# Kernel optimization log

Measured on AMD Instinct MI355X. Metric: run time of the kernel, lower is better.

Reference implementation:

```python
import jax, jax.numpy as jnp
import numpy as np

EMB_DIM = 256
N_EMBED = 1024
BETA = 0.25


def setup_inputs() -> dict:
    key = jax.random.key(0)
    k1, k2 = jax.random.split(key)
    encoderout = jax.random.normal(k1, (32, EMB_DIM, 32, 32), dtype=jnp.float32)
    # embedding.weight.data.normal_(mean=0, std=1/n_embed)
    codebook = jax.random.normal(k2, (N_EMBED, EMB_DIM), dtype=jnp.float32) * (1.0 / N_EMBED)
    return {"encoderout": encoderout, "codebook": codebook}


def reference(encoderout, codebook):
    # NCHW -> NHWC
    x = jnp.transpose(encoderout, (0, 2, 3, 1))  # [B,H,W,D]
    flat = x.reshape(-1, EMB_DIM)                # [N,D]
    d2 = (jnp.sum(flat * flat, axis=1, keepdims=True)
          + jnp.sum(codebook * codebook, axis=1)[None, :]
          - 2.0 * flat @ codebook.T)             # [N,K]
    idx = jnp.argmin(d2, axis=1)                 # [N]
    quant = codebook[idx].reshape(x.shape)       # [B,H,W,D]
    codebook_loss = jnp.mean((quant - jax.lax.stop_gradient(x)) ** 2)
    commitment_loss = jnp.mean((x - jax.lax.stop_gradient(quant)) ** 2)
    loss = codebook_loss + BETA * commitment_loss
    # FAITHFUL to source bug: straight-through output is overwritten by the
    # input permuted back to NCHW, so out == encoderout.
    out = jnp.transpose(x, (0, 3, 1, 2))
    return (out, loss, codebook_loss, commitment_loss)
```

## Files before the change

### kernel.cpp

```cpp
#include <hip/hip_runtime.h>
#include <stdint.h>

typedef short s8v __attribute__((ext_vector_type(8)));
typedef float f4v __attribute__((ext_vector_type(4)));

#define EMB_DIM 256
#define HW      1024
#define NROWS   32768
#define NELEM   (NROWS * EMB_DIM)

#define PK_OFF   0u
#define CBN_OFF  524288u
#define PSQ_OFF  528384u
#define PSM_OFF  530432u

__device__ __forceinline__ unsigned f2bf(float f) {
    union { float f; unsigned u; } c; c.f = f;
    unsigned u = c.u;
    return (u + 0x7FFFu + ((u >> 16) & 1u)) >> 16;
}

__global__ __launch_bounds__(256) void prep_cb(const float* __restrict__ cb,
                                               unsigned short* __restrict__ pk,
                                               float* __restrict__ cbn) {
    int T = blockIdx.x, t = threadIdx.x;
    {
        int code = t >> 4, seg = t & 15;
        const float* src = cb + (size_t)(T * 16 + code) * EMB_DIM + seg * 16;
        float s2 = 0.f;
        #pragma unroll
        for (int k = 0; k < 4; ++k) {
            float4 v = *(const float4*)(src + 4 * k);
            s2 += v.x * v.x + v.y * v.y + v.z * v.z + v.w * v.w;
        }
        #pragma unroll
        for (int m = 1; m < 16; m <<= 1) s2 += __shfl_xor(s2, m, 64);
        if (seg == 0) cbn[T * 16 + code] = s2;
    }
    #pragma unroll
    for (int it = 0; it < 2; ++it) {
        int idx = t + 256 * it;
        int s = idx >> 6, l = idx & 63, G = l >> 4, ci = l & 15;
        const float* q = cb + (size_t)(T * 16 + ci) * EMB_DIM + 32 * s + 8 * G;
        float4 v0 = *(const float4*)(q);
        float4 v1 = *(const float4*)(q + 4);
        unsigned o0 = f2bf(v0.x) | (f2bf(v0.y) << 16);
        unsigned o1 = f2bf(v0.z) | (f2bf(v0.w) << 16);
        unsigned o2 = f2bf(v1.x) | (f2bf(v1.y) << 16);
        unsigned o3 = f2bf(v1.z) | (f2bf(v1.w) << 16);
        *(uint4*)((char*)pk + (size_t)T * 8192 + (size_t)idx * 16) =
            make_uint4(o0, o1, o2, o3);
    }
}

__global__ __launch_bounds__(256, 2) void vq_fused(const float* __restrict__ x,
                                                   float* __restrict__ out,
                                                   const unsigned short* __restrict__ pk,
                                                   const float* __restrict__ cbn,
                                                   float* __restrict__ psq,
                                                   float* __restrict__ psm) {
    __shared__ float smemf[64 * 69];
    __shared__ uint4 frag[4 * 8 * 64];
    __shared__ float mloc[4][64];
    __shared__ float red[4];

    int t = threadIdx.x;
    int blk = blockIdx.x;
    int b = blk >> 4, p0 = (blk & 15) << 6;
    const float* xb = x   + (size_t)b * (EMB_DIM * HW) + p0;
    float*       ob = out + (size_t)b * (EMB_DIM * HW) + p0;

    int l = t & 63, w = t >> 6;
    int G = l >> 4, ci = l & 15;

    float sq = 0.f;
    int pq = t & 15, dd = t >> 4;
    for (int kd = 0; kd < 4; ++kd) {
        #pragma unroll
        for (int c2 = 0; c2 < 4; ++c2) {
            int dl = dd + 16 * c2;
            size_t off = (size_t)(kd * 64 + dl) * HW + 4 * pq;
            float4 v = *(const float4*)(xb + off);
            *(float4*)(ob + off) = v;
            sq += v.x * v.x + v.y * v.y + v.z * v.z + v.w * v.w;
            float* dst = &smemf[dl * 69 + 4 * pq];
            dst[0] = v.x; dst[1] = v.y; dst[2] = v.z; dst[3] = v.w;
        }
        __syncthreads();
        #pragma unroll
        for (int it = 0; it < 2; ++it) {
            int f = t + 256 * it;
            int fl = f & 63, sL = (f >> 6) & 1, R = f >> 7;
            int fG = fl >> 4, fci = fl & 15;
            const float* q = &smemf[(32 * sL + 8 * fG) * 69 + 16 * R + fci];
            unsigned o0 = f2bf(q[0])   | (f2bf(q[69])  << 16);
            unsigned o1 = f2bf(q[138]) | (f2bf(q[207]) << 16);
            unsigned o2 = f2bf(q[276]) | (f2bf(q[345]) << 16);
            unsigned o3 = f2bf(q[414]) | (f2bf(q[483]) << 16);
            frag[(R * 8 + 2 * kd + sL) * 64 + fl] = make_uint4(o0, o1, o2, o3);
        }
        __syncthreads();
    }
    #pragma unroll
    for (int m = 1; m < 64; m <<= 1) sq += __shfl_xor(sq, m, 64);
    if (l == 0) red[w] = sq;

    s8v a[4][8];
    #pragma unroll
    for (int R = 0; R < 4; ++R)
        #pragma unroll
        for (int s = 0; s < 8; ++s)
            a[R][s] = *(const s8v*)&frag[(R * 8 + s) * 64 + l];

    float mv[4][4];
    #pragma unroll
    for (int R = 0; R < 4; ++R)
        #pragma unroll
        for (int r = 0; r < 4; ++r) mv[R][r] = 1e30f;

    const char* pb = (const char*)pk + (size_t)(w * 16) * 8192 + (size_t)l * 16;
    #pragma unroll 2
    for (int T = 0; T < 16; ++T) {
        const char* pt = pb + (size_t)T * 8192;
        f4v ac0 = {0.f,0.f,0.f,0.f}, ac1 = {0.f,0.f,0.f,0.f};
        f4v ac2 = {0.f,0.f,0.f,0.f}, ac3 = {0.f,0.f,0.f,0.f};
        #pragma unroll
        for (int s = 0; s < 8; ++s) {
            s8v bf = *(const s8v*)(pt + s * 1024);
            ac0 = __builtin_amdgcn_mfma_f32_16x16x32_bf16(a[0][s], bf, ac0, 0, 0, 0);
            ac1 = __builtin_amdgcn_mfma_f32_16x16x32_bf16(a[1][s], bf, ac1, 0, 0, 0);
            ac2 = __builtin_amdgcn_mfma_f32_16x16x32_bf16(a[2][s], bf, ac2, 0, 0, 0);
            ac3 = __builtin_amdgcn_mfma_f32_16x16x32_bf16(a[3][s], bf, ac3, 0, 0, 0);
        }
        float cv = cbn[(w * 16 + T) * 16 + ci];
        #pragma unroll
        for (int r = 0; r < 4; ++r) {
            mv[0][r] = fminf(mv[0][r], cv - 2.f * ac0[r]);
            mv[1][r] = fminf(mv[1][r], cv - 2.f * ac1[r]);
            mv[2][r] = fminf(mv[2][r], cv - 2.f * ac2[r]);
            mv[3][r] = fminf(mv[3][r], cv - 2.f * ac3[r]);
        }
    }

    #pragma unroll
    for (int R = 0; R < 4; ++R)
        #pragma unroll
        for (int r = 0; r < 4; ++r) {
            float v = mv[R][r];
            #pragma unroll
            for (int m = 1; m < 16; m <<= 1) v = fminf(v, __shfl_xor(v, m, 64));
            mv[R][r] = v;
        }
    if (ci == 0) {
        #pragma unroll
        for (int R = 0; R < 4; ++R)
            #pragma unroll
            for (int r = 0; r < 4; ++r)
                mloc[w][16 * R + 4 * G + r] = mv[R][r];
    }
    __syncthreads();

    if (t < 64) {
        float m = fminf(fminf(mloc[0][t], mloc[1][t]),
                        fminf(mloc[2][t], mloc[3][t]));
        #pragma unroll
        for (int mm = 1; mm < 64; mm <<= 1) m += __shfl_xor(m, mm, 64);
        if (t == 0) {
            psm[blk] = m;
            psq[blk] = red[0] + red[1] + red[2] + red[3];
        }
    }
}

__global__ __launch_bounds__(512) void fin_kernel(const float* __restrict__ psm,
                                                  const float* __restrict__ psq,
                                                  float* __restrict__ out) {
    int t = threadIdx.x;
    double s = (double)psm[t] + (double)psq[t];
    #pragma unroll
    for (int m = 1; m < 64; m <<= 1) s += __shfl_xor(s, m, 64);
    __shared__ double ds[8];
    if ((t & 63) == 0) ds[t >> 6] = s;
    __syncthreads();
    if (t == 0) {
        double tot = 0.0;
        #pragma unroll
        for (int k = 0; k < 8; ++k) tot += ds[k];
        double cl = tot / (double)NELEM;
        out[NELEM + 0] = (float)(1.25 * cl);
        out[NELEM + 1] = (float)cl;
        out[NELEM + 2] = (float)cl;
    }
}

extern "C" void kernel_launch(void* const* d_in, const int* in_sizes, int n_in,
                              void* d_out, int out_size, void* d_ws, size_t ws_size,
                              hipStream_t stream) {
    const float* enc = (const float*)d_in[0];
    const float* cb  = (const float*)d_in[1];
    float* out = (float*)d_out;

    unsigned short* pk = (unsigned short*)((char*)d_ws + PK_OFF);
    float* cbn = (float*)((char*)d_ws + CBN_OFF);
    float* psq = (float*)((char*)d_ws + PSQ_OFF);
    float* psm = (float*)((char*)d_ws + PSM_OFF);

    prep_cb<<<64, 256, 0, stream>>>(cb, pk, cbn);
    vq_fused<<<512, 256, 0, stream>>>(enc, out, pk, cbn, psq, psm);
    fin_kernel<<<1, 512, 0, stream>>>(psm, psq, out);
}
```

Measured before the change: 108.0 us.

## Prefetch codebook tiles, stagger tile order, nontemporal copy, fuse final reduction

The codebook MFMA loop now double-buffers its B fragments, loading the next tile into registers while the current one is consumed. Each block starts at a different tile offset to spread L2 accesses. The input-to-output copy uses nontemporal loads and stores. The separate finalize kernel is replaced by a last-block-done atomic counter inside the main kernel, which removes one launch but adds register pressure and a fence/atomic per block.

```diff
diff --git a/kernel.cpp b/kernel.cpp
--- a/kernel.cpp
+++ b/kernel.cpp
@@ -13,6 +13,7 @@
 #define CBN_OFF  524288u
 #define PSQ_OFF  528384u
 #define PSM_OFF  530432u
+#define DONE_OFF 532480u
 
 __device__ __forceinline__ unsigned f2bf(float f) {
     union { float f; unsigned u; } c; c.f = f;
@@ -22,8 +23,10 @@
 
 __global__ __launch_bounds__(256) void prep_cb(const float* __restrict__ cb,
                                                unsigned short* __restrict__ pk,
-                                               float* __restrict__ cbn) {
+                                               float* __restrict__ cbn,
+                                               unsigned* __restrict__ done) {
     int T = blockIdx.x, t = threadIdx.x;
+    if (T == 0 && t == 0) *done = 0u;
     {
         int code = t >> 4, seg = t & 15;
         const float* src = cb + (size_t)(T * 16 + code) * EMB_DIM + seg * 16;
@@ -58,11 +61,14 @@
                                                    const unsigned short* __restrict__ pk,
                                                    const float* __restrict__ cbn,
                                                    float* __restrict__ psq,
-                                                   float* __restrict__ psm) {
+                                                   float* __restrict__ psm,
+                                                   unsigned* __restrict__ done) {
     __shared__ float smemf[64 * 69];
     __shared__ uint4 frag[4 * 8 * 64];
     __shared__ float mloc[4][64];
     __shared__ float red[4];
+    __shared__ bool  lastf;
+    __shared__ double dred[4];
 
     int t = threadIdx.x;
     int blk = blockIdx.x;
@@ -80,8 +86,8 @@
         for (int c2 = 0; c2 < 4; ++c2) {
             int dl = dd + 16 * c2;
             size_t off = (size_t)(kd * 64 + dl) * HW + 4 * pq;
-            float4 v = *(const float4*)(xb + off);
-            *(float4*)(ob + off) = v;
+            f4v v = __builtin_nontemporal_load((const f4v*)(xb + off));
+            __builtin_nontemporal_store(v, (f4v*)(ob + off));
             sq += v.x * v.x + v.y * v.y + v.z * v.z + v.w * v.w;
             float* dst = &smemf[dl * 69 + 4 * pq];
             dst[0] = v.x; dst[1] = v.y; dst[2] = v.z; dst[3] = v.w;
@@ -118,21 +124,33 @@
         #pragma unroll
         for (int r = 0; r < 4; ++r) mv[R][r] = 1e30f;
 
-    const char* pb = (const char*)pk + (size_t)(w * 16) * 8192 + (size_t)l * 16;
+    const char* lbase = (const char*)pk + (size_t)l * 16;
+    int qbase = w * 16;
+    int off = blk & 15;
+    s8v cur[8], nxt[8];
+    {
+        const char* pt = lbase + (size_t)(qbase + off) * 8192;
+        #pragma unroll
+        for (int s = 0; s < 8; ++s) cur[s] = *(const s8v*)(pt + (size_t)s * 1024);
+    }
     #pragma unroll 2
-    for (int T = 0; T < 16; ++T) {
-        const char* pt = pb + (size_t)T * 8192;
+    for (int i = 0; i < 16; ++i) {
+        int Tn = qbase + ((off + ((i + 1) & 15)) & 15);
+        const char* pn = lbase + (size_t)Tn * 8192;
+        #pragma unroll
+        for (int s = 0; s < 8; ++s) nxt[s] = *(const s8v*)(pn + (size_t)s * 1024);
+
         f4v ac0 = {0.f,0.f,0.f,0.f}, ac1 = {0.f,0.f,0.f,0.f};
         f4v ac2 = {0.f,0.f,0.f,0.f}, ac3 = {0.f,0.f,0.f,0.f};
         #pragma unroll
         for (int s = 0; s < 8; ++s) {
-            s8v bf = *(const s8v*)(pt + s * 1024);
-            ac0 = __builtin_amdgcn_mfma_f32_16x16x32_bf16(a[0][s], bf, ac0, 0, 0, 0);
-            ac1 = __builtin_amdgcn_mfma_f32_16x16x32_bf16(a[1][s], bf, ac1, 0, 0, 0);
-            ac2 = __builtin_amdgcn_mfma_f32_16x16x32_bf16(a[2][s], bf, ac2, 0, 0, 0);
-            ac3 = __builtin_amdgcn_mfma_f32_16x16x32_bf16(a[3][s], bf, ac3, 0, 0, 0);
-        }
-        float cv = cbn[(w * 16 + T) * 16 + ci];
+            ac0 = __builtin_amdgcn_mfma_f32_16x16x32_bf16(a[0][s], cur[s], ac0, 0, 0, 0);
+            ac1 = __builtin_amdgcn_mfma_f32_16x16x32_bf16(a[1][s], cur[s], ac1, 0, 0, 0);
+            ac2 = __builtin_amdgcn_mfma_f32_16x16x32_bf16(a[2][s], cur[s], ac2, 0, 0, 0);
+            ac3 = __builtin_amdgcn_mfma_f32_16x16x32_bf16(a[3][s], cur[s], ac3, 0, 0, 0);
+        }
+        int Tc = qbase + ((off + i) & 15);
+        float cv = cbn[Tc * 16 + ci];
         #pragma unroll
         for (int r = 0; r < 4; ++r) {
             mv[0][r] = fminf(mv[0][r], cv - 2.f * ac0[r]);
@@ -140,6 +158,8 @@
             mv[2][r] = fminf(mv[2][r], cv - 2.f * ac2[r]);
             mv[3][r] = fminf(mv[3][r], cv - 2.f * ac3[r]);
         }
+        #pragma unroll
+        for (int s = 0; s < 8; ++s) cur[s] = nxt[s];
     }
 
     #pragma unroll
@@ -166,30 +186,37 @@
         #pragma unroll
         for (int mm = 1; mm < 64; mm <<= 1) m += __shfl_xor(m, mm, 64);
         if (t == 0) {
-            psm[blk] = m;
-            psq[blk] = red[0] + red[1] + red[2] + red[3];
-        }
-    }
-}
-
-__global__ __launch_bounds__(512) void fin_kernel(const float* __restrict__ psm,
-                                                  const float* __restrict__ psq,
-                                                  float* __restrict__ out) {
-    int t = threadIdx.x;
-    double s = (double)psm[t] + (double)psq[t];
-    #pragma unroll
-    for (int m = 1; m < 64; m <<= 1) s += __shfl_xor(s, m, 64);
-    __shared__ double ds[8];
-    if ((t & 63) == 0) ds[t >> 6] = s;
+            __hip_atomic_store(&psm[blk], m, __ATOMIC_RELAXED, __HIP_MEMORY_SCOPE_AGENT);
+            __hip_atomic_store(&psq[blk], red[0] + red[1] + red[2] + red[3],
+                               __ATOMIC_RELAXED, __HIP_MEMORY_SCOPE_AGENT);
+            __threadfence();
+            unsigned old = __hip_atomic_fetch_add(done, 1u, __ATOMIC_RELAXED,
+                                                  __HIP_MEMORY_SCOPE_AGENT);
+            lastf = (old == 511u);
+        }
+    }
     __syncthreads();
-    if (t == 0) {
-        double tot = 0.0;
-        #pragma unroll
-        for (int k = 0; k < 8; ++k) tot += ds[k];
-        double cl = tot / (double)NELEM;
-        out[NELEM + 0] = (float)(1.25 * cl);
-        out[NELEM + 1] = (float)cl;
-        out[NELEM + 2] = (float)cl;
+
+    if (lastf) {
+        __threadfence();
+        double s = 0.0;
+        #pragma unroll
+        for (int h = 0; h < 2; ++h) {
+            int idx = t + 256 * h;
+            s += (double)__hip_atomic_load(&psm[idx], __ATOMIC_RELAXED, __HIP_MEMORY_SCOPE_AGENT)
+               + (double)__hip_atomic_load(&psq[idx], __ATOMIC_RELAXED, __HIP_MEMORY_SCOPE_AGENT);
+        }
+        #pragma unroll
+        for (int m = 1; m < 64; m <<= 1) s += __shfl_xor(s, m, 64);
+        if (l == 0) dred[w] = s;
+        __syncthreads();
+        if (t == 0) {
+            double tot = dred[0] + dred[1] + dred[2] + dred[3];
+            double cl = tot / (double)NELEM;
+            out[NELEM + 0] = (float)(1.25 * cl);
+            out[NELEM + 1] = (float)cl;
+            out[NELEM + 2] = (float)cl;
+        }
     }
 }
 
@@ -201,11 +228,11 @@
     float* out = (float*)d_out;
 
     unsigned short* pk = (unsigned short*)((char*)d_ws + PK_OFF);
-    float* cbn = (float*)((char*)d_ws + CBN_OFF);
-    float* psq = (float*)((char*)d_ws + PSQ_OFF);
-    float* psm = (float*)((char*)d_ws + PSM_OFF);
-
-    prep_cb<<<64, 256, 0, stream>>>(cb, pk, cbn);
-    vq_fused<<<512, 256, 0, stream>>>(enc, out, pk, cbn, psq, psm);
-    fin_kernel<<<1, 512, 0, stream>>>(psm, psq, out);
-}
+    float* cbn  = (float*)((char*)d_ws + CBN_OFF);
+    float* psq  = (float*)((char*)d_ws + PSQ_OFF);
+    float* psm  = (float*)((char*)d_ws + PSM_OFF);
+    unsigned* done = (unsigned*)((char*)d_ws + DONE_OFF);
+
+    prep_cb<<<64, 256, 0, stream>>>(cb, pk, cbn, done);
+    vq_fused<<<512, 256, 0, stream>>>(enc, out, pk, cbn, psq, psm, done);
+}
```

Result: slower. 115.8 us (+7.3%).
